# Kernel optimization log

Measured on AMD Instinct MI355X. Metric: run time of the kernel, lower is better.

Reference implementation:

```python
import jax, jax.numpy as jnp
import numpy as np

NUM_CLASS = 4
EMB_SIZE = 2048
S = 16.0


def setup_inputs() -> dict:
    key = jax.random.key(0)
    k1, k2, k3 = jax.random.split(key, 3)
    fea = jax.random.normal(k1, (16384, EMB_SIZE), dtype=jnp.float32)
    # nn.Linear default init: U(-1/sqrt(fan_in), 1/sqrt(fan_in))
    bound = 1.0 / np.sqrt(EMB_SIZE)
    W = jax.random.uniform(k2, (NUM_CLASS, EMB_SIZE), dtype=jnp.float32, minval=-bound, maxval=bound)
    b = jax.random.uniform(k3, (NUM_CLASS,), dtype=jnp.float32, minval=-bound, maxval=bound)
    return {"fea": fea, "W": W, "b": b}


def reference(fea, W, b):
    # L2 normalize along axis=1 (torch.norm(p=2, dim=1, keepdim=True); no eps)
    norm = jnp.sqrt(jnp.sum(fea * fea, axis=1, keepdims=True))  # [B, 1]
    fea_n = fea / norm
    # Linear: y = x @ W^T + b, then scalar scale
    logit = (jnp.einsum('be,ce->bc', fea_n, W) + b) * S  # [B, num_class]
    return logit
```

## Files before the change

kernel.cpp:

```cpp
#include <hip/hip_runtime.h>

#define EMB 2048
#define NC 4
#define NROWS 16384
#define SCALE_S 16.0f

#define ROWS_PER_WAVE 4
#define WAVES_PER_BLOCK 4
#define ROWS_PER_BLOCK (ROWS_PER_WAVE * WAVES_PER_BLOCK)

__global__ __launch_bounds__(256) void binary_head_kernel(
    const float* __restrict__ fea,
    const float* __restrict__ W,
    const float* __restrict__ bias,
    float* __restrict__ out)
{
    __shared__ float4 sW[NC * (EMB / 4)];

    const int tid = threadIdx.x;

    const float4* W4 = (const float4*)W;
#pragma unroll
    for (int i = 0; i < 8; ++i) {
        sW[i * 256 + tid] = W4[i * 256 + tid];
    }

    const int wave = tid >> 6;
    const int lane = tid & 63;

    const float bval = bias[lane & (NC - 1)];

    const float4* fea4 = (const float4*)fea;
    const int rowBase = blockIdx.x * ROWS_PER_BLOCK + wave * ROWS_PER_WAVE;

    float4 x[8], xn[8];
    {
        const float4* frow = fea4 + (size_t)rowBase * (EMB / 4);
#pragma unroll
        for (int j = 0; j < 8; ++j) {
            x[j] = frow[j * 64 + lane];
        }
    }

    __syncthreads();

#pragma unroll
    for (int r = 0; r < ROWS_PER_WAVE; ++r) {
        if (r + 1 < ROWS_PER_WAVE) {
            const float4* fnext = fea4 + (size_t)(rowBase + r + 1) * (EMB / 4);
#pragma unroll
            for (int j = 0; j < 8; ++j) {
                xn[j] = fnext[j * 64 + lane];
            }
        }

        float ss = 0.0f, d0 = 0.0f, d1 = 0.0f, d2 = 0.0f, d3 = 0.0f;
#pragma unroll
        for (int j = 0; j < 8; ++j) {
            const float4 v = x[j];
            const int col = j * 64 + lane;

            ss += v.x * v.x + v.y * v.y + v.z * v.z + v.w * v.w;

            const float4 w0 = sW[0 * 512 + col];
            d0 += v.x * w0.x + v.y * w0.y + v.z * w0.z + v.w * w0.w;
            const float4 w1 = sW[1 * 512 + col];
            d1 += v.x * w1.x + v.y * w1.y + v.z * w1.z + v.w * w1.w;
            const float4 w2 = sW[2 * 512 + col];
            d2 += v.x * w2.x + v.y * w2.y + v.z * w2.z + v.w * w2.w;
            const float4 w3 = sW[3 * 512 + col];
            d3 += v.x * w3.x + v.y * w3.y + v.z * w3.z + v.w * w3.w;
        }

#pragma unroll
        for (int m = 1; m < 64; m <<= 1) {
            ss += __shfl_xor(ss, m, 64);
            d0 += __shfl_xor(d0, m, 64);
            d1 += __shfl_xor(d1, m, 64);
            d2 += __shfl_xor(d2, m, 64);
            d3 += __shfl_xor(d3, m, 64);
        }

        const int row = rowBase + r;
        if (lane < NC) {
            const float d = (lane == 0) ? d0 : (lane == 1) ? d1 : (lane == 2) ? d2 : d3;
            const float inv = rsqrtf(ss);
            out[row * NC + lane] = (d * inv + bval) * SCALE_S;
        }

        if (r + 1 < ROWS_PER_WAVE) {
#pragma unroll
            for (int j = 0; j < 8; ++j) {
                x[j] = xn[j];
            }
        }
    }
}

extern "C" void kernel_launch(void* const* d_in, const int* in_sizes, int n_in,
                              void* d_out, int out_size, void* d_ws, size_t ws_size,
                              hipStream_t stream) {
    const float* fea  = (const float*)d_in[0];
    const float* W    = (const float*)d_in[1];
    const float* bias = (const float*)d_in[2];
    float* out = (float*)d_out;

    const int grid = NROWS / ROWS_PER_BLOCK;
    binary_head_kernel<<<grid, 256, 0, stream>>>(fea, W, bias, out);
}
```

Before: 189.7 us.

## Process rows in groups of four per wave with batched loads and reductions

Each wave now handles 8 rows in two groups of 4, loading all 4 rows of a group at once so more memory requests are in flight. Each shared-memory weight fetch is reused across the 4 rows, and the next group's loads are issued before the cross-lane reduction of the current group. The launch bound now asks for 2 blocks per CU, which caps registers, and the grid has half as many blocks. The larger register footprint (32 float4 live) risks spills or lower occupancy.

```diff
diff --git a/kernel.cpp b/kernel.cpp
--- a/kernel.cpp
+++ b/kernel.cpp
@@ -5,11 +5,12 @@
 #define NROWS 16384
 #define SCALE_S 16.0f
 
-#define ROWS_PER_WAVE 4
+#define RG 4
+#define NG 2
 #define WAVES_PER_BLOCK 4
-#define ROWS_PER_BLOCK (ROWS_PER_WAVE * WAVES_PER_BLOCK)
+#define ROWS_PER_BLOCK (RG * NG * WAVES_PER_BLOCK)
 
-__global__ __launch_bounds__(256) void binary_head_kernel(
+__global__ __launch_bounds__(256, 2) void binary_head_kernel(
     const float* __restrict__ fea,
     const float* __restrict__ W,
     const float* __restrict__ bias,
@@ -31,67 +32,76 @@
     const float bval = bias[lane & (NC - 1)];
 
     const float4* fea4 = (const float4*)fea;
-    const int rowBase = blockIdx.x * ROWS_PER_BLOCK + wave * ROWS_PER_WAVE;
+    const int waveRowBase = blockIdx.x * ROWS_PER_BLOCK + wave * (RG * NG);
 
-    float4 x[8], xn[8];
-    {
-        const float4* frow = fea4 + (size_t)rowBase * (EMB / 4);
+    float4 x[RG][8];
+#pragma unroll
+    for (int r = 0; r < RG; ++r) {
+        const float4* frow = fea4 + (size_t)(waveRowBase + r) * (EMB / 4);
 #pragma unroll
         for (int j = 0; j < 8; ++j) {
-            x[j] = frow[j * 64 + lane];
+            x[r][j] = frow[j * 64 + lane];
         }
     }
 
     __syncthreads();
 
 #pragma unroll
-    for (int r = 0; r < ROWS_PER_WAVE; ++r) {
-        if (r + 1 < ROWS_PER_WAVE) {
-            const float4* fnext = fea4 + (size_t)(rowBase + r + 1) * (EMB / 4);
+    for (int g = 0; g < NG; ++g) {
+        float ss[RG] = {0.0f, 0.0f, 0.0f, 0.0f};
+        float d[RG][NC] = {};
+
 #pragma unroll
-            for (int j = 0; j < 8; ++j) {
-                xn[j] = fnext[j * 64 + lane];
+        for (int j = 0; j < 8; ++j) {
+            const int col = j * 64 + lane;
+            const float4 w0 = sW[0 * 512 + col];
+            const float4 w1 = sW[1 * 512 + col];
+            const float4 w2 = sW[2 * 512 + col];
+            const float4 w3 = sW[3 * 512 + col];
+#pragma unroll
+            for (int r = 0; r < RG; ++r) {
+                const float4 v = x[r][j];
+                ss[r]   += v.x * v.x  + v.y * v.y  + v.z * v.z  + v.w * v.w;
+                d[r][0] += v.x * w0.x + v.y * w0.y + v.z * w0.z + v.w * w0.w;
+                d[r][1] += v.x * w1.x + v.y * w1.y + v.z * w1.z + v.w * w1.w;
+                d[r][2] += v.x * w2.x + v.y * w2.y + v.z * w2.z + v.w * w2.w;
+                d[r][3] += v.x * w3.x + v.y * w3.y + v.z * w3.z + v.w * w3.w;
             }
         }
 
-        float ss = 0.0f, d0 = 0.0f, d1 = 0.0f, d2 = 0.0f, d3 = 0.0f;
+        if (g + 1 < NG) {
+            const int nb = waveRowBase + (g + 1) * RG;
 #pragma unroll
-        for (int j = 0; j < 8; ++j) {
-            const float4 v = x[j];
-            const int col = j * 64 + lane;
-
-            ss += v.x * v.x + v.y * v.y + v.z * v.z + v.w * v.w;
-
-            const float4 w0 = sW[0 * 512 + col];
-            d0 += v.x * w0.x + v.y * w0.y + v.z * w0.z + v.w * w0.w;
-            const float4 w1 = sW[1 * 512 + col];
-            d1 += v.x * w1.x + v.y * w1.y + v.z * w1.z + v.w * w1.w;
-            const float4 w2 = sW[2 * 512 + col];
-            d2 += v.x * w2.x + v.y * w2.y + v.z * w2.z + v.w * w2.w;
-            const float4 w3 = sW[3 * 512 + col];
-            d3 += v.x * w3.x + v.y * w3.y + v.z * w3.z + v.w * w3.w;
+            for (int r = 0; r < RG; ++r) {
+                const float4* frow = fea4 + (size_t)(nb + r) * (EMB / 4);
+#pragma unroll
+                for (int j = 0; j < 8; ++j) {
+                    x[r][j] = frow[j * 64 + lane];
+                }
+            }
         }
 
 #pragma unroll
         for (int m = 1; m < 64; m <<= 1) {
-            ss += __shfl_xor(ss, m, 64);
-            d0 += __shfl_xor(d0, m, 64);
-            d1 += __shfl_xor(d1, m, 64);
-            d2 += __shfl_xor(d2, m, 64);
-            d3 += __shfl_xor(d3, m, 64);
+#pragma unroll
+            for (int r = 0; r < RG; ++r) {
+                ss[r]   += __shfl_xor(ss[r],   m, 64);
+                d[r][0] += __shfl_xor(d[r][0], m, 64);
+                d[r][1] += __shfl_xor(d[r][1], m, 64);
+                d[r][2] += __shfl_xor(d[r][2], m, 64);
+                d[r][3] += __shfl_xor(d[r][3], m, 64);
+            }
         }
 
-        const int row = rowBase + r;
+        const int row0 = waveRowBase + g * RG;
         if (lane < NC) {
-            const float d = (lane == 0) ? d0 : (lane == 1) ? d1 : (lane == 2) ? d2 : d3;
-            const float inv = rsqrtf(ss);
-            out[row * NC + lane] = (d * inv + bval) * SCALE_S;
-        }
-
-        if (r + 1 < ROWS_PER_WAVE) {
 #pragma unroll
-            for (int j = 0; j < 8; ++j) {
-                x[j] = xn[j];
+            for (int r = 0; r < RG; ++r) {
+                const float dv = (lane == 0) ? d[r][0]
+                               : (lane == 1) ? d[r][1]
+                               : (lane == 2) ? d[r][2]
+                               :               d[r][3];
+                out[(row0 + r) * NC + lane] = (dv * rsqrtf(ss[r]) + bval) * SCALE_S;
             }
         }
     }
```

Measured after the change: 195.1 us. 1.03x slower.
